# Optimization experiments

Measured on AMD Instinct MI355X. Metric: run time of the kernel, lower is better.

Reference implementation:

```python
import jax, jax.numpy as jnp
import numpy as np

N_NODES = 100000
EPS = 1e-5


def gcn_conv(x, edge_index, W, b):
    # PyG GCNConv: add self loops, symmetric normalization, aggregate at target.
    n = x.shape[0]
    xw = x @ W                                  # [N, F_out]
    loop = jnp.arange(n)
    src = jnp.concatenate([edge_index[0], loop])
    dst = jnp.concatenate([edge_index[1], loop])
    deg = jax.ops.segment_sum(jnp.ones_like(dst, dtype=xw.dtype), dst, num_segments=n)
    dinv = jnp.where(deg > 0, jax.lax.rsqrt(deg), 0.0)
    norm = dinv[src] * dinv[dst]                # [E+N]
    out = jax.ops.segment_sum(norm[:, None] * xw[src], dst, num_segments=n)
    return out + b


def batch_norm(x, gamma, beta):
    # training-mode BatchNorm1d over node dim
    m = x.mean(axis=0)
    v = x.var(axis=0)
    return (x - m) * jax.lax.rsqrt(v + EPS) * gamma + beta


def setup_inputs() -> dict:
    key = jax.random.key(0)
    ks = jax.random.split(key, 16)
    dims = [(128, 256), (256, 128), (128, 64)]
    inp = {
        "x": jax.random.normal(ks[0], (N_NODES, 128), dtype=jnp.float32),
        "edge_index": jax.random.randint(ks[1], (2, 1600000), 0, N_NODES),
        "pos_edge_index": jax.random.randint(ks[2], (2, 200000), 0, N_NODES),
        "neg_edge_index": jax.random.randint(ks[3], (2, 200000), 0, N_NODES),
    }
    for i, (fi, fo) in enumerate(dims, start=1):
        inp[f"W{i}"] = jax.random.normal(ks[3 + i], (fi, fo), dtype=jnp.float32) / np.sqrt(fi)
        inp[f"b{i}"] = jnp.zeros((fo,), dtype=jnp.float32)
        inp[f"g{i}"] = jnp.ones((fo,), dtype=jnp.float32)
        inp[f"beta{i}"] = jnp.zeros((fo,), dtype=jnp.float32)
    return inp


def reference(x, edge_index, pos_edge_index, neg_edge_index,
              W1, b1, g1, beta1, W2, b2, g2, beta2, W3, b3, g3, beta3):
    # encode
    h = gcn_conv(x, edge_index, W1, b1)
    h = jax.nn.sigmoid(batch_norm(h, g1, beta1))
    h = gcn_conv(h, edge_index, W2, b2)
    h = jax.nn.sigmoid(batch_norm(h, g2, beta2))
    h = gcn_conv(h, edge_index, W3, b3)
    z = batch_norm(h, g3, beta3)                # [N, 64]
    # decode
    ei = jnp.concatenate([pos_edge_index, neg_edge_index], axis=-1)
    logits = jnp.sum(z[ei[0]] * z[ei[1]], axis=-1)
    return logits
```

## Files before the change

### kernel.cpp

```cpp
#include <hip/hip_runtime.h>
#include <hip/hip_bf16.h>
#include <stddef.h>


#define WAVE 64
#define BSHIFT 9
#define SCHUNK 4096

typedef __attribute__((ext_vector_type(8))) short short8;
typedef __attribute__((ext_vector_type(4))) float f32x4;

__device__ __forceinline__ float bl(uint g) { return __uint_as_float(g << 16); }
__device__ __forceinline__ float bh(uint g) { return __uint_as_float(g & 0xffff0000u); }
__device__ __forceinline__ ushort f2b(float f) {
    uint u = __float_as_uint(f);
    return (ushort)((u + 0x7fffu + ((u >> 16) & 1u)) >> 16);
}
__device__ __forceinline__ uint pack2(float lo, float hi) {
    return (uint)f2b(lo) | ((uint)f2b(hi) << 16);
}

__global__ __launch_bounds__(256) void k_bhist(const int* __restrict__ dst, int* __restrict__ gh, int E) {
    __shared__ int lh[256];
    lh[threadIdx.x] = 0; __syncthreads();
    int i = blockIdx.x * 256 + threadIdx.x, stride = gridDim.x * 256;
    for (; i < E; i += stride) atomicAdd(&lh[dst[i] >> BSHIFT], 1);
    __syncthreads();
    int v = lh[threadIdx.x];
    if (v) atomicAdd(&gh[threadIdx.x], v);
}

__global__ void k_bscan(const int* __restrict__ gh, int* __restrict__ boff, int* __restrict__ bcur) {
    __shared__ int ls[256];
    int t = threadIdx.x;
    int v = gh[t];
    ls[t] = v; __syncthreads();
    for (int off = 1; off < 256; off <<= 1) {
        int x = (t >= off) ? ls[t - off] : 0;
        __syncthreads();
        ls[t] += x;
        __syncthreads();
    }
    int excl = ls[t] - v;
    boff[t] = excl; bcur[t] = excl;
    if (t == 255) boff[256] = ls[255];
}

__global__ __launch_bounds__(256) void k_bscatter(const int* __restrict__ src, const int* __restrict__ dst,
                                                  int* __restrict__ gcur, int2* __restrict__ pairs, int E) {
    __shared__ int lh[256];
    int t = threadIdx.x;
    int base = blockIdx.x * SCHUNK;
    lh[t] = 0; __syncthreads();
    int rs[16], rd[16];
    #pragma unroll
    for (int i = 0; i < 16; ++i) {
        int idx = base + i * 256 + t;
        if (idx < E) { rs[i] = src[idx]; rd[i] = dst[idx]; atomicAdd(&lh[rd[i] >> BSHIFT], 1); }
        else rd[i] = -1;
    }
    __syncthreads();
    int cnt_b = lh[t];
    int b0 = cnt_b ? atomicAdd(&gcur[t], cnt_b) : 0;
    lh[t] = b0;
    __syncthreads();
    #pragma unroll
    for (int i = 0; i < 16; ++i) {
        if (rd[i] >= 0) {
            int p = atomicAdd(&lh[rd[i] >> BSHIFT], 1);
            pairs[p] = make_int2(rs[i], rd[i]);
        }
    }
}

__global__ __launch_bounds__(256) void k_bfine(const int2* __restrict__ pairs, const int* __restrict__ boff,
                                               int* __restrict__ rowptr, int* __restrict__ srcs,
                                               float* __restrict__ dinv, int N, int E) {
    __shared__ int lcnt[512];
    __shared__ int ls[256];
    int b = blockIdx.x, t = threadIdx.x;
    int d0 = b << BSHIFT;
    int e0 = boff[b], e1 = boff[b + 1];
    lcnt[t] = 0; lcnt[t + 256] = 0;
    __syncthreads();
    for (int e = e0 + t; e < e1; e += 256)
        atomicAdd(&lcnt[pairs[e].y - d0], 1);
    __syncthreads();
    int c0 = lcnt[2 * t], c1 = lcnt[2 * t + 1];
    ls[t] = c0 + c1;
    __syncthreads();
    for (int off = 1; off < 256; off <<= 1) {
        int x = (t >= off) ? ls[t - off] : 0;
        __syncthreads();
        ls[t] += x;
        __syncthreads();
    }
    int excl = ls[t] - (c0 + c1);
    int s0 = excl, s1 = excl + c0;
    int d = d0 + 2 * t;
    if (d < N)     { rowptr[d] = e0 + s0;     dinv[d] = rsqrtf((float)(c0 + 1)); }
    if (d + 1 < N) { rowptr[d + 1] = e0 + s1; dinv[d + 1] = rsqrtf((float)(c1 + 1)); }
    if (b == 0 && t == 0) rowptr[N] = E;
    lcnt[2 * t] = s0; lcnt[2 * t + 1] = s1;
    __syncthreads();
    for (int e = e0 + t; e < e1; e += 256) {
        int2 p = pairs[e];
        int pos = atomicAdd(&lcnt[p.y - d0], 1);
        srcs[e0 + pos] = p.x;
    }
}

__global__ void k_convx(const float* __restrict__ in, ushort* __restrict__ out, size_t n4) {
    size_t i = (size_t)blockIdx.x * blockDim.x + threadIdx.x;
    if (i >= n4) return;
    float4 v = reinterpret_cast<const float4*>(in)[i];
    uint2 o;
    o.x = pack2(v.x, v.y);
    o.y = pack2(v.z, v.w);
    reinterpret_cast<uint2*>(out)[i] = o;
}

__global__ void k_convWT(const float* __restrict__ W, ushort* __restrict__ Wt, int K, int N) {
    int i = blockIdx.x * blockDim.x + threadIdx.x;
    if (i >= K * N) return;
    int k = i / N, n = i % N;
    Wt[(size_t)n * K + k] = f2b(W[i]);
}

template<int F>
__global__ __launch_bounds__(256) void k_agg(const ushort* __restrict__ in, ushort* __restrict__ out,
                                             const int* __restrict__ rowptr, const int* __restrict__ srcs,
                                             const float* __restrict__ dinv, int N) {
    constexpr int L = (F * 2) / 16;
    int wv = threadIdx.x >> 6, lane = threadIdx.x & 63;
    int node = (blockIdx.x * 4 + wv) * (64 / L) + lane / L;
    int sl = lane % L;
    if (node >= N) return;
    const uint4* inq = reinterpret_cast<const uint4*>(in);
    float di = dinv[node];
    float acc[8];
    {
        uint4 v = inq[(size_t)node * L + sl];
        acc[0] = di * bl(v.x); acc[1] = di * bh(v.x);
        acc[2] = di * bl(v.y); acc[3] = di * bh(v.y);
        acc[4] = di * bl(v.z); acc[5] = di * bh(v.z);
        acc[6] = di * bl(v.w); acc[7] = di * bh(v.w);
    }
    int e = rowptr[node], e1 = rowptr[node + 1];
    for (; e + 1 < e1; e += 2) {
        int s0 = srcs[e], s1 = srcs[e + 1];
        float d0 = dinv[s0], d1 = dinv[s1];
        uint4 v0 = inq[(size_t)s0 * L + sl];
        uint4 v1 = inq[(size_t)s1 * L + sl];
        acc[0] += d0 * bl(v0.x) + d1 * bl(v1.x);
        acc[1] += d0 * bh(v0.x) + d1 * bh(v1.x);
        acc[2] += d0 * bl(v0.y) + d1 * bl(v1.y);
        acc[3] += d0 * bh(v0.y) + d1 * bh(v1.y);
        acc[4] += d0 * bl(v0.z) + d1 * bl(v1.z);
        acc[5] += d0 * bh(v0.z) + d1 * bh(v1.z);
        acc[6] += d0 * bl(v0.w) + d1 * bl(v1.w);
        acc[7] += d0 * bh(v0.w) + d1 * bh(v1.w);
    }
    if (e < e1) {
        int s0 = srcs[e];
        float d0 = dinv[s0];
        uint4 v0 = inq[(size_t)s0 * L + sl];
        acc[0] += d0 * bl(v0.x); acc[1] += d0 * bh(v0.x);
        acc[2] += d0 * bl(v0.y); acc[3] += d0 * bh(v0.y);
        acc[4] += d0 * bl(v0.z); acc[5] += d0 * bh(v0.z);
        acc[6] += d0 * bl(v0.w); acc[7] += d0 * bh(v0.w);
    }
    uint4 o;
    o.x = pack2(acc[0] * di, acc[1] * di);
    o.y = pack2(acc[2] * di, acc[3] * di);
    o.z = pack2(acc[4] * di, acc[5] * di);
    o.w = pack2(acc[6] * di, acc[7] * di);
    reinterpret_cast<uint4*>(out)[(size_t)node * L + sl] = o;
}

template<int F>
__global__ __launch_bounds__(256) void k_bnstats(const ushort* __restrict__ h, float* __restrict__ gsum,
                                                 float* __restrict__ gsq, int N) {
    constexpr int C = F / 8;
    constexpr int RPW = 64 / C;
    __shared__ float ls[4][16][16];
    int wv = threadIdx.x >> 6, lane = threadIdx.x & 63;
    int fidx = lane % C, rsub = lane / C;
    int row = (blockIdx.x * 4 + wv) * RPW + rsub;
    int rstride = gridDim.x * 4 * RPW;
    const uint4* hq = reinterpret_cast<const uint4*>(h);
    float s[8] = {}, q[8] = {};
    for (int r = row; r < N; r += rstride) {
        uint4 v = hq[(size_t)r * C + fidx];
        float x;
        x = bl(v.x); s[0] += x; q[0] += x * x;
        x = bh(v.x); s[1] += x; q[1] += x * x;
        x = bl(v.y); s[2] += x; q[2] += x * x;
        x = bh(v.y); s[3] += x; q[3] += x * x;
        x = bl(v.z); s[4] += x; q[4] += x * x;
        x = bh(v.z); s[5] += x; q[5] += x * x;
        x = bl(v.w); s[6] += x; q[6] += x * x;
        x = bh(v.w); s[7] += x; q[7] += x * x;
    }
    #pragma unroll
    for (int m = C; m < 64; m <<= 1) {
        #pragma unroll
        for (int j = 0; j < 8; ++j) { s[j] += __shfl_xor(s[j], m); q[j] += __shfl_xor(q[j], m); }
    }
    if (lane < C) {
        #pragma unroll
        for (int j = 0; j < 8; ++j) { ls[wv][lane][j] = s[j]; ls[wv][lane][8 + j] = q[j]; }
    }
    __syncthreads();
    int t = threadIdx.x;
    if (t < F) {
        int ch = t / 8, j = t % 8;
        float S = 0.f, Q = 0.f;
        #pragma unroll
        for (int w = 0; w < 4; ++w) { S += ls[w][ch][j]; Q += ls[w][ch][8 + j]; }
        atomicAdd(&gsum[t], S); atomicAdd(&gsq[t], Q);
    }
}

template<int K, int NF, bool APPLY, bool STATS>
__global__ __launch_bounds__(256) void k_mfma(const ushort* __restrict__ A, const ushort* __restrict__ Wt,
                                              ushort* __restrict__ C, int M, int Nout,
                                              const float* __restrict__ sc, const float* __restrict__ sh,
                                              float* __restrict__ gsum, float* __restrict__ gsq) {
    int m0 = blockIdx.x * 128;
    int n0 = blockIdx.y * (NF * 32);
    int w = threadIdx.x >> 6, lane = threadIdx.x & 63;
    int wr = w >> 1, wc = w & 1;
    int rf = lane & 15;
    int kg = lane >> 4;

    const ushort* ap[4];
    #pragma unroll
    for (int mf = 0; mf < 4; ++mf) {
        int row = m0 + wr * 64 + mf * 16 + rf;
        if (row >= M) row = M - 1;
        ap[mf] = A + (size_t)row * K + kg * 8;
    }
    const ushort* bp[NF];
    #pragma unroll
    for (int nf = 0; nf < NF; ++nf)
        bp[nf] = Wt + (size_t)(n0 + wc * (NF * 16) + nf * 16 + rf) * K + kg * 8;

    f32x4 acc[4][NF];
    #pragma unroll
    for (int mf = 0; mf < 4; ++mf)
        #pragma unroll
        for (int nf = 0; nf < NF; ++nf)
            acc[mf][nf] = (f32x4){0.f, 0.f, 0.f, 0.f};

    #pragma unroll 2
    for (int kk = 0; kk < K / 32; ++kk) {
        short8 a[4], b[NF];
        #pragma unroll
        for (int mf = 0; mf < 4; ++mf) {
            a[mf] = *reinterpret_cast<const short8*>(ap[mf] + kk * 32);
            if constexpr (APPLY) {
                int kbase = kk * 32 + kg * 8;
                union { short8 s; uint u[4]; } in, o;
                in.s = a[mf];
                #pragma unroll
                for (int i = 0; i < 4; ++i) {
                    int k = kbase + 2 * i;
                    float x0 = bl(in.u[i]) * sc[k] + sh[k];
                    float x1 = bh(in.u[i]) * sc[k + 1] + sh[k + 1];
                    x0 = 1.f / (1.f + __expf(-x0));
                    x1 = 1.f / (1.f + __expf(-x1));
                    o.u[i] = pack2(x0, x1);
                }
                a[mf] = o.s;
            }
        }
        #pragma unroll
        for (int nf = 0; nf < NF; ++nf)
            b[nf] = *reinterpret_cast<const short8*>(bp[nf] + kk * 32);
        #pragma unroll
        for (int mf = 0; mf < 4; ++mf)
            #pragma unroll
            for (int nf = 0; nf < NF; ++nf)
                acc[mf][nf] = __builtin_amdgcn_mfma_f32_16x16x32_bf16(a[mf], b[nf], acc[mf][nf], 0, 0, 0);
    }

    #pragma unroll
    for (int mf = 0; mf < 4; ++mf)
        #pragma unroll
        for (int nf = 0; nf < NF; ++nf) {
            int col = n0 + wc * (NF * 16) + nf * 16 + rf;
            #pragma unroll
            for (int j = 0; j < 4; ++j) {
                int row = m0 + wr * 64 + mf * 16 + kg * 4 + j;
                if (row < M) C[(size_t)row * Nout + col] = f2b(acc[mf][nf][j]);
            }
        }

    if constexpr (STATS) {
        __shared__ float bns[2][NF * 32], bnq[2][NF * 32];
        #pragma unroll
        for (int nf = 0; nf < NF; ++nf) {
            float cs = 0.f, cq = 0.f;
            #pragma unroll
            for (int mf = 0; mf < 4; ++mf)
                #pragma unroll
                for (int j = 0; j < 4; ++j) {
                    int row = m0 + wr * 64 + mf * 16 + kg * 4 + j;
                    float v = (row < M) ? acc[mf][nf][j] : 0.f;
                    cs += v; cq += v * v;
                }
            cs += __shfl_xor(cs, 16); cs += __shfl_xor(cs, 32);
            cq += __shfl_xor(cq, 16); cq += __shfl_xor(cq, 32);
            if (kg == 0) { bns[wr][wc * (NF * 16) + nf * 16 + rf] = cs; bnq[wr][wc * (NF * 16) + nf * 16 + rf] = cq; }
        }
        __syncthreads();
        int t = threadIdx.x;
        if (t < NF * 32) {
            atomicAdd(&gsum[n0 + t], bns[0][t] + bns[1][t]);
            atomicAdd(&gsq[n0 + t],  bnq[0][t] + bnq[1][t]);
        }
    }
}

__global__ void k_bnfin(const float* __restrict__ sums, const float* __restrict__ sumsq,
                        const float* __restrict__ g, const float* __restrict__ beta,
                        float* __restrict__ scale, float* __restrict__ shift, int F, float invN) {
    int f = threadIdx.x;
    if (f < F) {
        float m = sums[f] * invN;
        float var = sumsq[f] * invN - m * m;
        float s = g[f] * rsqrtf(var + 1e-5f);
        scale[f] = s;
        shift[f] = beta[f] - m * s;
    }
}

__global__ __launch_bounds__(256) void k_decode(const ushort* __restrict__ h,
                                                const float* __restrict__ sc, const float* __restrict__ sh,
                                                const int* __restrict__ pos, const int* __restrict__ neg,
                                                int Pp, int Pn, float* __restrict__ out) {
    int gid = blockIdx.x * 16 + (threadIdx.x >> 4);
    int l = threadIdx.x & 15;
    int P = Pp + Pn;
    if (gid >= P) return;
    int a, b;
    if (gid < Pp) { a = pos[gid]; b = pos[Pp + gid]; }
    else          { int e = gid - Pp; a = neg[e]; b = neg[Pn + e]; }
    const uint2* hu = reinterpret_cast<const uint2*>(h);
    uint2 ua = hu[(size_t)a * 16 + l];
    uint2 ub = hu[(size_t)b * 16 + l];
    int f = l * 4;
    float s0 = sc[f], s1 = sc[f + 1], s2 = sc[f + 2], s3 = sc[f + 3];
    float t0 = sh[f], t1 = sh[f + 1], t2 = sh[f + 2], t3 = sh[f + 3];
    float a0 = bl(ua.x) * s0 + t0, a1 = bh(ua.x) * s1 + t1, a2 = bl(ua.y) * s2 + t2, a3 = bh(ua.y) * s3 + t3;
    float b0 = bl(ub.x) * s0 + t0, b1 = bh(ub.x) * s1 + t1, b2 = bl(ub.y) * s2 + t2, b3 = bh(ub.y) * s3 + t3;
    float d = a0 * b0 + a1 * b1 + a2 * b2 + a3 * b3;
    d += __shfl_xor(d, 1);
    d += __shfl_xor(d, 2);
    d += __shfl_xor(d, 4);
    d += __shfl_xor(d, 8);
    if (l == 0) out[gid] = d;
}

extern "C" void kernel_launch(void* const* d_in, const int* in_sizes, int n_in,
                              void* d_out, int out_size, void* d_ws, size_t ws_size,
                              hipStream_t stream) {
    const float* x   = (const float*)d_in[0];
    const int*   ei  = (const int*)d_in[1];
    const int*   pe  = (const int*)d_in[2];
    const int*   ne  = (const int*)d_in[3];
    const float* W1  = (const float*)d_in[4];
    const float* g1  = (const float*)d_in[6];
    const float* be1 = (const float*)d_in[7];
    const float* W2  = (const float*)d_in[8];
    const float* g2  = (const float*)d_in[10];
    const float* be2 = (const float*)d_in[11];
    const float* W3  = (const float*)d_in[12];
    const float* g3  = (const float*)d_in[14];
    const float* be3 = (const float*)d_in[15];
    float* out = (float*)d_out;

    const int N  = in_sizes[0] / 128;
    const int E  = in_sizes[1] / 2;
    const int Pp = in_sizes[2] / 2;
    const int Pn = in_sizes[3] / 2;

    char* ws = (char*)d_ws;
    auto carve = [&](size_t bytes) -> char* {
        char* p = ws;
        ws += (bytes + 255) & ~(size_t)255;
        return p;
    };
    char*  zz     = carve(256 * 4 + 896 * 4);
    int*   gh     = (int*)zz;
    float* sums1  = (float*)(zz + 1024);
    float* sq1    = sums1 + 256;
    float* sums2  = sq1 + 256;
    float* sq2    = sums2 + 128;
    float* sums3  = sq2 + 128;
    float* sq3    = sums3 + 64;
    size_t zz_bytes = 1024 + 896 * 4;

    int*    boff   = (int*)carve(257 * 4);
    int*    bcur   = (int*)carve(256 * 4);
    int*    rowptr = (int*)carve((size_t)(N + 1) * 4);
    float*  dinv   = (float*)carve((size_t)N * 4);
    int*    srcs   = (int*)carve((size_t)E * 4);
    int2*   pairs  = (int2*)carve((size_t)E * 8);
    float*  scale1 = (float*)carve(256 * 4);
    float*  shift1 = (float*)carve(256 * 4);
    float*  scale2 = (float*)carve(128 * 4);
    float*  shift2 = (float*)carve(128 * 4);
    float*  scale3 = (float*)carve(64 * 4);
    float*  shift3 = (float*)carve(64 * 4);
    ushort* Wt1    = (ushort*)carve(128 * 256 * 2);
    ushort* Wt2    = (ushort*)carve(256 * 128 * 2);
    ushort* Wt3    = (ushort*)carve(128 * 64 * 2);
    ushort* b1     = (ushort*)carve((size_t)N * 128 * 2);
    ushort* b2     = (ushort*)carve((size_t)N * 128 * 2);
    ushort* b3     = (ushort*)carve((size_t)N * 256 * 2);

    const int* e_src = ei;
    const int* e_dst = ei + E;
    const int NBUCK = (N + (1 << BSHIFT) - 1) >> BSHIFT;

    hipMemsetAsync(zz, 0, zz_bytes, stream);

    k_bhist<<<2048, 256, 0, stream>>>(e_dst, gh, E);
    k_bscan<<<1, 256, 0, stream>>>(gh, boff, bcur);
    k_bscatter<<<(E + SCHUNK - 1) / SCHUNK, 256, 0, stream>>>(e_src, e_dst, bcur, pairs, E);
    k_bfine<<<NBUCK, 256, 0, stream>>>(pairs, boff, rowptr, srcs, dinv, N, E);

    {
        size_t n4 = (size_t)N * 128 / 4;
        k_convx<<<(int)((n4 + 255) / 256), 256, 0, stream>>>(x, b1, n4);
        k_convWT<<<(128 * 256 + 255) / 256, 256, 0, stream>>>(W1, Wt1, 128, 256);
        k_convWT<<<(256 * 128 + 255) / 256, 256, 0, stream>>>(W2, Wt2, 256, 128);
        k_convWT<<<(128 * 64 + 255) / 256, 256, 0, stream>>>(W3, Wt3, 128, 64);
    }

    const int mblk = (N + 127) / 128;
    const int agg128 = (N + 15) / 16;
    const int agg64  = (N + 31) / 32;

    k_agg<128><<<agg128, 256, 0, stream>>>(b1, b2, rowptr, srcs, dinv, N);
    { dim3 g(mblk, 2); k_mfma<128, 4, false, true><<<g, 256, 0, stream>>>(b2, Wt1, b3, N, 256, nullptr, nullptr, sums1, sq1); }
    k_bnfin<<<1, 256, 0, stream>>>(sums1, sq1, g1, be1, scale1, shift1, 256, 1.0f / N);

    { dim3 g(mblk, 1); k_mfma<256, 4, true, false><<<g, 256, 0, stream>>>(b3, Wt2, b1, N, 128, scale1, shift1, nullptr, nullptr); }
    k_agg<128><<<agg128, 256, 0, stream>>>(b1, b2, rowptr, srcs, dinv, N);
    k_bnstats<128><<<512, 256, 0, stream>>>(b2, sums2, sq2, N);
    k_bnfin<<<1, 256, 0, stream>>>(sums2, sq2, g2, be2, scale2, shift2, 128, 1.0f / N);

    { dim3 g(mblk, 1); k_mfma<128, 2, true, false><<<g, 256, 0, stream>>>(b2, Wt3, b1, N, 64, scale2, shift2, nullptr, nullptr); }
    k_agg<64><<<agg64, 256, 0, stream>>>(b1, b2, rowptr, srcs, dinv, N);
    k_bnstats<64><<<512, 256, 0, stream>>>(b2, sums3, sq3, N);
    k_bnfin<<<1, 256, 0, stream>>>(sums3, sq3, g3, be3, scale3, shift3, 64, 1.0f / N);

    k_decode<<<(Pp + Pn + 15) / 16, 256, 0, stream>>>(b2, scale3, shift3, pe, ne, Pp, Pn, out);
}
```

Measured before the change: 580.9 us.

## Stage A tiles through swizzled LDS with register prefetch in MFMA GEMM

The MFMA GEMM now loads each 128x64 A tile cooperatively into shared memory with an XOR swizzle, prefetching the next k-slab into registers while computing on the current one. When the BN-apply plus sigmoid transform is fused in, it runs once per element at staging time instead of in every wave that reads the element, and scale/shift are cached in LDS. The aim is to cut redundant global A loads and duplicated transcendental work across the two column waves. The cost is two block barriers per k-slab and extra LDS use.

```diff
diff --git a/kernel.cpp b/kernel.cpp
--- a/kernel.cpp
+++ b/kernel.cpp
@@ -227,20 +227,34 @@
                                               ushort* __restrict__ C, int M, int Nout,
                                               const float* __restrict__ sc, const float* __restrict__ sh,
                                               float* __restrict__ gsum, float* __restrict__ gsq) {
+    constexpr int S = K / 64;
+    __shared__ uint4 Alds[128 * 8];
+    __shared__ float scl[K], shl[K];
     int m0 = blockIdx.x * 128;
     int n0 = blockIdx.y * (NF * 32);
-    int w = threadIdx.x >> 6, lane = threadIdx.x & 63;
+    int t = threadIdx.x;
+    int w = t >> 6, lane = t & 63;
     int wr = w >> 1, wc = w & 1;
-    int rf = lane & 15;
-    int kg = lane >> 4;
-
-    const ushort* ap[4];
-    #pragma unroll
-    for (int mf = 0; mf < 4; ++mf) {
-        int row = m0 + wr * 64 + mf * 16 + rf;
-        if (row >= M) row = M - 1;
-        ap[mf] = A + (size_t)row * K + kg * 8;
-    }
+    int rf = lane & 15, kg = lane >> 4;
+
+    if (APPLY) {
+        for (int i = t; i < K; i += 256) { scl[i] = sc[i]; shl[i] = sh[i]; }
+    }
+
+    int srow[4], schk[4];
+    const ushort* sga[4];
+    #pragma unroll
+    for (int i = 0; i < 4; ++i) {
+        int chunk = t + i * 256;
+        int r = chunk >> 3, c = chunk & 7;
+        srow[i] = r; schk[i] = c;
+        int gr = m0 + r; if (gr >= M) gr = M - 1;
+        sga[i] = A + (size_t)gr * K + c * 8;
+    }
+    uint4 regs[4];
+    #pragma unroll
+    for (int i = 0; i < 4; ++i) regs[i] = *reinterpret_cast<const uint4*>(sga[i]);
+
     const ushort* bp[NF];
     #pragma unroll
     for (int nf = 0; nf < NF; ++nf)
@@ -253,36 +267,53 @@
         for (int nf = 0; nf < NF; ++nf)
             acc[mf][nf] = (f32x4){0.f, 0.f, 0.f, 0.f};
 
-    #pragma unroll 2
-    for (int kk = 0; kk < K / 32; ++kk) {
-        short8 a[4], b[NF];
-        #pragma unroll
-        for (int mf = 0; mf < 4; ++mf) {
-            a[mf] = *reinterpret_cast<const short8*>(ap[mf] + kk * 32);
+    if (APPLY) __syncthreads();
+
+    for (int s = 0; s < S; ++s) {
+        #pragma unroll
+        for (int i = 0; i < 4; ++i) {
+            uint4 v = regs[i];
             if constexpr (APPLY) {
-                int kbase = kk * 32 + kg * 8;
-                union { short8 s; uint u[4]; } in, o;
-                in.s = a[mf];
+                uint u[4] = {v.x, v.y, v.z, v.w};
+                int kb = s * 64 + schk[i] * 8;
                 #pragma unroll
-                for (int i = 0; i < 4; ++i) {
-                    int k = kbase + 2 * i;
-                    float x0 = bl(in.u[i]) * sc[k] + sh[k];
-                    float x1 = bh(in.u[i]) * sc[k + 1] + sh[k + 1];
+                for (int j = 0; j < 4; ++j) {
+                    int k = kb + 2 * j;
+                    float x0 = bl(u[j]) * scl[k] + shl[k];
+                    float x1 = bh(u[j]) * scl[k + 1] + shl[k + 1];
                     x0 = 1.f / (1.f + __expf(-x0));
                     x1 = 1.f / (1.f + __expf(-x1));
-                    o.u[i] = pack2(x0, x1);
+                    u[j] = pack2(x0, x1);
                 }
-                a[mf] = o.s;
+                v.x = u[0]; v.y = u[1]; v.z = u[2]; v.w = u[3];
             }
-        }
-        #pragma unroll
-        for (int nf = 0; nf < NF; ++nf)
-            b[nf] = *reinterpret_cast<const short8*>(bp[nf] + kk * 32);
-        #pragma unroll
-        for (int mf = 0; mf < 4; ++mf)
+            Alds[srow[i] * 8 + (schk[i] ^ (srow[i] & 7))] = v;
+        }
+        if (s + 1 < S) {
+            #pragma unroll
+            for (int i = 0; i < 4; ++i)
+                regs[i] = *reinterpret_cast<const uint4*>(sga[i] + (s + 1) * 64);
+        }
+        __syncthreads();
+        #pragma unroll
+        for (int kk = 0; kk < 2; ++kk) {
+            short8 a[4], b[NF];
+            #pragma unroll
+            for (int mf = 0; mf < 4; ++mf) {
+                int R = wr * 64 + mf * 16 + rf;
+                a[mf] = *reinterpret_cast<const short8*>(&Alds[R * 8 + ((kk * 4 + kg) ^ (R & 7))]);
+            }
+            int kglob = s * 64 + kk * 32;
             #pragma unroll
             for (int nf = 0; nf < NF; ++nf)
-                acc[mf][nf] = __builtin_amdgcn_mfma_f32_16x16x32_bf16(a[mf], b[nf], acc[mf][nf], 0, 0, 0);
+                b[nf] = *reinterpret_cast<const short8*>(bp[nf] + kglob);
+            #pragma unroll
+            for (int mf = 0; mf < 4; ++mf)
+                #pragma unroll
+                for (int nf = 0; nf < NF; ++nf)
+                    acc[mf][nf] = __builtin_amdgcn_mfma_f32_16x16x32_bf16(a[mf], b[nf], acc[mf][nf], 0, 0, 0);
+        }
+        __syncthreads();
     }
 
     #pragma unroll
@@ -315,7 +346,6 @@
             if (kg == 0) { bns[wr][wc * (NF * 16) + nf * 16 + rf] = cs; bnq[wr][wc * (NF * 16) + nf * 16 + rf] = cq; }
         }
         __syncthreads();
-        int t = threadIdx.x;
         if (t < NF * 32) {
             atomicAdd(&gsum[n0 + t], bns[0][t] + bns[1][t]);
             atomicAdd(&gsq[n0 + t],  bnq[0][t] + bnq[1][t]);
```

Result: faster. 549.7 us (-5.4%).
